# Performance work log

Measured on AMD Instinct MI355X. Metric: run time of the kernel, lower is better.

The kernel has to match this reference:

```python
import jax, jax.numpy as jnp
import numpy as np

TAU = 2.0
BN_EPS = 1e-5


def ms_lif(x_seq, v_th):
    # Multi-step LIF: v <- v + (x - v)/tau; spike = H(v - v_th); hard reset to 0.
    def step(v, x):
        v = v + (x - v) / TAU
        s = (v >= v_th).astype(x.dtype)
        v = v * (1.0 - s)
        return v, s
    _, spikes = jax.lax.scan(step, jnp.zeros_like(x_seq[0]), x_seq)
    return spikes


def conv1x1(x, w):
    # x: [TB, C, H, W], w: [O, C]
    return jnp.einsum('bchw,oc->bohw', x, w)


def bn(x, gamma, beta, mean, var):
    scale = gamma / jnp.sqrt(var + BN_EPS)
    shift = beta - mean * scale
    return x * scale[None, :, None, None] + shift[None, :, None, None]


def setup_inputs() -> dict:
    key = jax.random.key(0)
    ks = jax.random.split(key, 20)
    T, B, C, H, W = 4, 32, 384, 16, 16
    d = {'x': jax.random.normal(ks[0], (T, B, C, H, W), jnp.float32)}
    def bn_params(i):
        return (jax.random.uniform(ks[i], (C,), jnp.float32, 0.5, 1.5),
                jax.random.normal(ks[i + 1], (C,), jnp.float32) * 0.1,
                jax.random.normal(ks[i + 2], (C,), jnp.float32) * 0.1,
                jax.random.uniform(ks[i + 3], (C,), jnp.float32, 0.5, 1.5))
    d['q_w'] = jax.random.normal(ks[1], (C, C), jnp.float32) * (C ** -0.5)
    d['q_gamma'], d['q_beta'], d['q_mean'], d['q_var'] = bn_params(2)
    d['k_w'] = jax.random.normal(ks[6], (C, C), jnp.float32) * (C ** -0.5)
    d['k_gamma'], d['k_beta'], d['k_mean'], d['k_var'] = bn_params(7)
    d['v_w'] = jax.random.normal(ks[11], (C, C), jnp.float32) * (C ** -0.5)
    d['v_gamma'], d['v_beta'], d['v_mean'], d['v_var'] = bn_params(12)
    d['proj_w'] = jax.random.normal(ks[16], (C, C), jnp.float32) * (C ** -0.5)
    d['proj_b'] = jnp.zeros((C,), jnp.float32)
    d['proj_gamma'], d['proj_beta'], d['proj_mean'], d['proj_var'] = bn_params(16)
    return d


def reference(x, q_w, q_gamma, q_beta, q_mean, q_var,
              k_w, k_gamma, k_beta, k_mean, k_var,
              v_w, v_gamma, v_beta, v_mean, v_var,
              proj_w, proj_b, proj_gamma, proj_beta, proj_mean, proj_var):
    T, B, C, H, W = x.shape
    nh = 8
    dh = C // nh
    N = H * W
    identity = x
    xs = ms_lif(x, 1.0)                        # shortcut_lif
    xf = xs.reshape(T * B, C, H, W)

    def branch(w, g, b, m, v_):
        y = bn(conv1x1(xf, w), g, b, m, v_).reshape(T, B, C, H, W)
        return ms_lif(y, 1.0)

    def to_heads(s):  # [T,B,C,H,W] -> [T,B,nh,N,dh]
        return s.reshape(T, B, C, N).transpose(0, 1, 3, 2).reshape(T, B, N, nh, dh).transpose(0, 1, 3, 2, 4)

    q = to_heads(branch(q_w, q_gamma, q_beta, q_mean, q_var))
    k = to_heads(branch(k_w, k_gamma, k_beta, k_mean, k_var))
    v = to_heads(branch(v_w, v_gamma, v_beta, v_mean, v_var))

    kv = (k * v).sum(axis=-2, keepdims=True)   # [T,B,nh,1,dh]
    kv = ms_lif(kv, 0.5)                       # talking_heads_lif (v_th=0.5)
    y = q * kv                                 # [T,B,nh,N,dh]
    y = y.transpose(0, 1, 2, 4, 3).reshape(T * B, C, H, W)
    out = conv1x1(y, proj_w) + proj_b[None, :, None, None]
    out = bn(out, proj_gamma, proj_beta, proj_mean, proj_var).reshape(T, B, C, H, W)
    out = out + identity
    return out, v
```

## Files before the change

### kernel.cpp

```cpp
#include <hip/hip_runtime.h>

#define T_ 4
#define B_ 32
#define C_ 384
#define N_ 256
#define NH_ 8
#define DH_ 48
#define CG_ 48
#define WELE_ 147456
#define FRAGS_M_ 442368
#define ELEMS_ ((size_t)T_*B_*C_*N_)

typedef __bf16 bf16x8 __attribute__((ext_vector_type(8)));
typedef float  f32x4  __attribute__((ext_vector_type(4)));
typedef unsigned int u32x4 __attribute__((ext_vector_type(4)));
typedef unsigned int u32x2 __attribute__((ext_vector_type(2)));
typedef unsigned short u16;

__device__ __forceinline__ float bf2f(u16 h){
  unsigned u = ((unsigned)h) << 16;
  return __builtin_bit_cast(float, u);
}
__device__ __forceinline__ u16 f2bf(float f){
  unsigned u = __builtin_bit_cast(unsigned, f);
  u += 0x7FFFu + ((u >> 16) & 1u);
  return (u16)(u >> 16);
}

__global__ __launch_bounds__(256) void k0_split(
    const float* __restrict__ wq, const float* __restrict__ wk,
    const float* __restrict__ wv, const float* __restrict__ wp,
    u16* __restrict__ ws)
{
  const int m = blockIdx.y;
  const int tid = blockIdx.x * 256 + threadIdx.x;
  const float* W = (m == 0) ? wq : (m == 1) ? wk : (m == 2) ? wv : wp;
  const int fo   = tid / 768;
  const int rem  = tid % 768;
  const int k32  = rem / 64;
  const int lane = rem % 64;
  const int row  = fo*16 + (lane & 15);
  const int col  = k32*32 + (lane >> 4)*8;
  const float* src = W + (size_t)row*C_ + col;

  u16 hi8[8], mi8[8], lo8[8];
#pragma unroll
  for (int e = 0; e < 8; e++){
    float w = src[e];
    u16 hi = f2bf(w);  float r1 = w  - bf2f(hi);
    u16 mi = f2bf(r1); float r2 = r1 - bf2f(mi);
    u16 lo = f2bf(r2);
    hi8[e] = hi; mi8[e] = mi; lo8[e] = lo;
  }
  u16* dst = ws + (size_t)m*FRAGS_M_ + (size_t)((fo*12 + k32)*3)*512 + (size_t)lane*8;
  u32x4 pk;
#pragma unroll
  for (int p = 0; p < 3; p++){
    const u16* s = (p == 0) ? hi8 : (p == 1) ? mi8 : lo8;
    pk[0] = (unsigned)s[0] | ((unsigned)s[1] << 16);
    pk[1] = (unsigned)s[2] | ((unsigned)s[3] << 16);
    pk[2] = (unsigned)s[4] | ((unsigned)s[5] << 16);
    pk[3] = (unsigned)s[6] | ((unsigned)s[7] << 16);
    *(u32x4*)(dst + (size_t)p*512) = pk;
  }
}

__global__ __launch_bounds__(256) void k1_lif_in(const float* __restrict__ x, u16* __restrict__ xs)
{
  const int b = blockIdx.x, cg = blockIdx.y, n = threadIdx.x;
  const int c0 = cg * 8;
  float v[8];
#pragma unroll
  for (int i = 0; i < 8; i++) v[i] = 0.f;
#pragma unroll
  for (int t = 0; t < T_; t++){
    const float* xp = x + (((size_t)(t*B_ + b))*C_ + c0)*N_ + n;
    u16 sp[8];
#pragma unroll
    for (int i = 0; i < 8; i++){
      float xv = xp[(size_t)i * N_];
      float vv = v[i] + (xv - v[i]) * 0.5f;
      bool s = vv >= 1.0f;
      sp[i] = s ? (u16)0x3F80u : (u16)0u;
      v[i] = s ? 0.f : vv;
    }
    u32x4 pk;
    pk[0] = (unsigned)sp[0] | ((unsigned)sp[1] << 16);
    pk[1] = (unsigned)sp[2] | ((unsigned)sp[3] << 16);
    pk[2] = (unsigned)sp[4] | ((unsigned)sp[5] << 16);
    pk[3] = (unsigned)sp[6] | ((unsigned)sp[7] << 16);
    *(u32x4*)(xs + ((size_t)((t*B_ + b)*CG_ + cg))*2048 + (size_t)n*8) = pk;
  }
}

__global__ __launch_bounds__(256) void k2_branch(
    const u16* __restrict__ xs, const u16* __restrict__ wsplit,
    const float* __restrict__ gq, const float* __restrict__ beq, const float* __restrict__ mq, const float* __restrict__ vaq,
    const float* __restrict__ gk, const float* __restrict__ bek, const float* __restrict__ mk, const float* __restrict__ vak,
    const float* __restrict__ gv, const float* __restrict__ bev, const float* __restrict__ mv, const float* __restrict__ vav,
    u16* __restrict__ qspk, u16* __restrict__ kspk, u16* __restrict__ vspk)
{
  const int id   = blockIdx.x;
  const int xcd  = id & 7;
  const int rest = id >> 3;
  const int obi  = rest % 18;
  const int nb4  = (rest / 18) & 3;
  const int bloc = rest / 72;
  const int b    = xcd * 4 + bloc;
  const int ob   = obi * 64;
  const int nb   = nb4 * 64;

  const int lane = threadIdx.x & 63;
  const int w    = __builtin_amdgcn_readfirstlane((int)(threadIdx.x >> 6));
  const int wo = w & 1, wn = w >> 1;
  const int l15 = lane & 15, lg = lane >> 4;
  const int branch = ob / C_;
  const int obr = (ob % C_) + wo * 32;
  const int fo  = obr >> 4;

  const float *G, *Be, *M, *Va; u16* spdst;
  if (branch == 0){ G=gq; Be=beq; M=mq; Va=vaq; spdst=qspk; }
  else if (branch == 1){ G=gk; Be=bek; M=mk; Va=vak; spdst=kspk; }
  else { G=gv; Be=bev; M=mv; Va=vav; spdst=vspk; }

  const int nbl = nb + wn * 32;

  const u16* wb0 = wsplit + (size_t)branch*FRAGS_M_ + (size_t)(fo*36)*512;
  const u16* wb1 = wb0 + (size_t)36*512;
  const u16* xb0 = xs + (size_t)((0*B_ + b)*CG_)*2048;
  const u16* xb1 = xs + (size_t)((1*B_ + b)*CG_)*2048;
  const u16* xb2 = xs + (size_t)((2*B_ + b)*CG_)*2048;
  const u16* xb3 = xs + (size_t)((3*B_ + b)*CG_)*2048;
  const unsigned woff = (unsigned)lane * 8;
  const unsigned xoff = (unsigned)(lg*2048 + (nbl + l15)*8);

  f32x4 acc[T_][2][2];
#pragma unroll
  for (int t = 0; t < T_; t++)
#pragma unroll
    for (int io = 0; io < 2; io++)
#pragma unroll
      for (int in = 0; in < 2; in++) acc[t][io][in] = (f32x4){0.f,0.f,0.f,0.f};

#pragma unroll
  for (int k = 0; k < 12; k++){
    bf16x8 wf[2][3];
    wf[0][0] = *(const bf16x8*)(wb0 + woff);
    wf[0][1] = *(const bf16x8*)(wb0 + woff + 512);
    wf[0][2] = *(const bf16x8*)(wb0 + woff + 1024);
    wf[1][0] = *(const bf16x8*)(wb1 + woff);
    wf[1][1] = *(const bf16x8*)(wb1 + woff + 512);
    wf[1][2] = *(const bf16x8*)(wb1 + woff + 1024);

    bf16x8 bb[T_][2];
    bb[0][0] = *(const bf16x8*)(xb0 + xoff);
    bb[0][1] = *(const bf16x8*)(xb0 + xoff + 128);
    bb[1][0] = *(const bf16x8*)(xb1 + xoff);
    bb[1][1] = *(const bf16x8*)(xb1 + xoff + 128);
    bb[2][0] = *(const bf16x8*)(xb2 + xoff);
    bb[2][1] = *(const bf16x8*)(xb2 + xoff + 128);
    bb[3][0] = *(const bf16x8*)(xb3 + xoff);
    bb[3][1] = *(const bf16x8*)(xb3 + xoff + 128);

#pragma unroll
    for (int t = 0; t < T_; t++)
#pragma unroll
      for (int in = 0; in < 2; in++){
        acc[t][0][in] = __builtin_amdgcn_mfma_f32_16x16x32_bf16(wf[0][2], bb[t][in], acc[t][0][in], 0, 0, 0);
        acc[t][0][in] = __builtin_amdgcn_mfma_f32_16x16x32_bf16(wf[0][1], bb[t][in], acc[t][0][in], 0, 0, 0);
        acc[t][0][in] = __builtin_amdgcn_mfma_f32_16x16x32_bf16(wf[0][0], bb[t][in], acc[t][0][in], 0, 0, 0);
        acc[t][1][in] = __builtin_amdgcn_mfma_f32_16x16x32_bf16(wf[1][2], bb[t][in], acc[t][1][in], 0, 0, 0);
        acc[t][1][in] = __builtin_amdgcn_mfma_f32_16x16x32_bf16(wf[1][1], bb[t][in], acc[t][1][in], 0, 0, 0);
        acc[t][1][in] = __builtin_amdgcn_mfma_f32_16x16x32_bf16(wf[1][0], bb[t][in], acc[t][1][in], 0, 0, 0);
      }

    wb0 += 1536; wb1 += 1536;
    xb0 += 8192; xb1 += 8192; xb2 += 8192; xb3 += 8192;
  }

  float sc[2][4], sh[2][4];
#pragma unroll
  for (int io = 0; io < 2; io++)
#pragma unroll
    for (int j = 0; j < 4; j++){
      int o = obr + io*16 + lg*4 + j;
      float s = G[o] / sqrtf(Va[o] + 1e-5f);
      sc[io][j] = s;
      sh[io][j] = Be[o] - __fmul_rn(M[o], s);
    }

  float vm[2][2][4];
#pragma unroll
  for (int io = 0; io < 2; io++)
#pragma unroll
    for (int in = 0; in < 2; in++)
#pragma unroll
      for (int j = 0; j < 4; j++) vm[io][in][j] = 0.f;

#pragma unroll
  for (int t = 0; t < T_; t++){
#pragma unroll
    for (int io = 0; io < 2; io++)
#pragma unroll
      for (int in = 0; in < 2; in++){
        int n = nbl + in*16 + l15;
        u16 sp[4];
#pragma unroll
        for (int j = 0; j < 4; j++){
          float z = __fadd_rn(__fmul_rn(acc[t][io][in][j], sc[io][j]), sh[io][j]);
          float vv = vm[io][in][j];
          vv = vv + (z - vv) * 0.5f;
          bool s = vv >= 1.0f;
          sp[j] = s ? (u16)0x3F80u : (u16)0u;
          vm[io][in][j] = s ? 0.f : vv;
        }
        u32x2 pk;
        pk[0] = (unsigned)sp[0] | ((unsigned)sp[1] << 16);
        pk[1] = (unsigned)sp[2] | ((unsigned)sp[3] << 16);
        int od = obr + io*16 + lg*4;
        u16* dst = spdst + (size_t)((t*B_ + b)*CG_ + (od >> 3))*2048 + (size_t)n*8 + (od & 7);
        *(u32x2*)dst = pk;
      }
  }
}

__global__ __launch_bounds__(256) void k3_kv(
    const u16* __restrict__ kspk, const u16* __restrict__ vspk, u16* __restrict__ kvm)
{
  const int wid  = (int)((blockIdx.x * blockDim.x + threadIdx.x) >> 6);
  const int lane = threadIdx.x & 63;
  const int b = wid / CG_, cg = wid % CG_;
  float u[8];
#pragma unroll
  for (int i = 0; i < 8; i++) u[i] = 0.f;

#pragma unroll
  for (int t = 0; t < T_; t++){
    int cnt[8];
#pragma unroll
    for (int i = 0; i < 8; i++) cnt[i] = 0;
    const size_t rowoff = (size_t)((t*B_ + b)*CG_ + cg)*2048;
    const u16* kp = kspk + rowoff;
    const u16* vp = vspk + rowoff;
#pragma unroll
    for (int j = 0; j < 4; j++){
      int n = j*64 + lane;
      u32x4 kk = *(const u32x4*)(kp + (size_t)n*8);
      u32x4 vv = *(const u32x4*)(vp + (size_t)n*8);
#pragma unroll
      for (int wd = 0; wd < 4; wd++){
        unsigned both = kk[wd] & vv[wd];
        cnt[2*wd]   += (both & 0xFFFFu) ? 1 : 0;
        cnt[2*wd+1] += (both >> 16)     ? 1 : 0;
      }
    }
#pragma unroll
    for (int i = 0; i < 8; i++){
#pragma unroll
      for (int off = 32; off >= 1; off >>= 1) cnt[i] += __shfl_xor(cnt[i], off, 64);
    }
    u16 mk[8];
#pragma unroll
    for (int i = 0; i < 8; i++){
      float kvf = (float)cnt[i];
      float uu = u[i] + (kvf - u[i]) * 0.5f;
      bool s = uu >= 0.5f;
      mk[i] = s ? (u16)0xFFFFu : (u16)0u;
      u[i] = s ? 0.f : uu;
    }
    if (lane == 0){
      u32x4 pk;
      pk[0] = (unsigned)mk[0] | ((unsigned)mk[1] << 16);
      pk[1] = (unsigned)mk[2] | ((unsigned)mk[3] << 16);
      pk[2] = (unsigned)mk[4] | ((unsigned)mk[5] << 16);
      pk[3] = (unsigned)mk[6] | ((unsigned)mk[7] << 16);
      *(u32x4*)(kvm + (size_t)(t*B_ + b)*C_ + cg*8) = pk;
    }
  }
}

__global__ __launch_bounds__(256) void k5_vtrans(const u16* __restrict__ vspk, float* __restrict__ vout)
{
  const int tb = blockIdx.x, h = blockIdx.y;
  const u16* src = vspk + ((size_t)tb*CG_ + h*6)*2048;
  float* dst = vout + ((size_t)tb*NH_ + h)*(N_*DH_);
#pragma unroll
  for (int i = 0; i < 12; i++){
    int f = i*1024 + threadIdx.x*4;
    int n = f / DH_;
    int d = f - n*DH_;
    u32x2 rv = *(const u32x2*)(src + (size_t)(d >> 3)*2048 + (size_t)n*8 + (d & 7));
    f32x4 o;
    o[0] = (rv[0] & 0xFFFFu) ? 1.f : 0.f;
    o[1] = (rv[0] >> 16)     ? 1.f : 0.f;
    o[2] = (rv[1] & 0xFFFFu) ? 1.f : 0.f;
    o[3] = (rv[1] >> 16)     ? 1.f : 0.f;
    *(f32x4*)(dst + f) = o;
  }
}

__global__ __launch_bounds__(256) void k4_proj(
    const u16* __restrict__ qspk, const u16* __restrict__ kvm, const u16* __restrict__ wsplit,
    const float* __restrict__ pb,
    const float* __restrict__ gp, const float* __restrict__ bep,
    const float* __restrict__ mp, const float* __restrict__ vap,
    const float* __restrict__ x, float* __restrict__ out)
{
  const int id   = blockIdx.x;
  const int xcd  = id & 7;
  const int rest = id >> 3;
  const int obi  = rest % 6;
  const int nb2  = (rest / 6) & 1;
  const int tbl  = rest / 12;
  const int tb   = xcd * 16 + tbl;
  const int ob   = obi * 64;
  const int nb   = nb2 * 128;

  __shared__ __align__(16) u16 kvmask[C_];
  for (int i = threadIdx.x; i < C_; i += 256) kvmask[i] = kvm[(size_t)tb*C_ + i];
  __syncthreads();

  const int lane = threadIdx.x & 63;
  const int w    = __builtin_amdgcn_readfirstlane((int)(threadIdx.x >> 6));
  const int wo = w & 1, wn = w >> 1;
  const int l15 = lane & 15, lg = lane >> 4;
  const int obw = ob + wo * 32;
  const int fo  = obw >> 4;
  const int nbl = nb + wn * 64;

  const u16* wb0 = wsplit + (size_t)3*FRAGS_M_ + (size_t)(fo*36)*512;
  const u16* wb1 = wb0 + (size_t)36*512;
  const u16* qb  = qspk + (size_t)(tb*CG_)*2048;
  const unsigned woff = (unsigned)lane * 8;
  const unsigned qoff = (unsigned)(lg*2048 + (nbl + l15)*8);

  float sc[2][4], sh[2][4], pbv[2][4];
#pragma unroll
  for (int io = 0; io < 2; io++)
#pragma unroll
    for (int j = 0; j < 4; j++){
      int o = obw + io*16 + lg*4 + j;
      float s = gp[o] / sqrtf(vap[o] + 1e-5f);
      sc[io][j] = s;
      sh[io][j] = bep[o] - __fmul_rn(mp[o], s);
      pbv[io][j] = pb[o];
    }

  f32x4 acc[2][4];
#pragma unroll
  for (int io = 0; io < 2; io++)
#pragma unroll
    for (int in = 0; in < 4; in++) acc[io][in] = (f32x4){0.f,0.f,0.f,0.f};

#pragma unroll
  for (int k = 0; k < 12; k++){
    bf16x8 a0 = *(const bf16x8*)(wb0 + woff);
    bf16x8 a1 = *(const bf16x8*)(wb1 + woff);
    u32x4 mv = *(const u32x4*)&kvmask[k*32 + lg*8];
    bf16x8 bb[4];
#pragma unroll
    for (int in = 0; in < 4; in++){
      u32x4 qv = *(const u32x4*)(qb + qoff + in*128);
      u32x4 yv = qv & mv;
      bb[in] = __builtin_bit_cast(bf16x8, yv);
    }
#pragma unroll
    for (int in = 0; in < 4; in++){
      acc[0][in] = __builtin_amdgcn_mfma_f32_16x16x32_bf16(a0, bb[in], acc[0][in], 0, 0, 0);
      acc[1][in] = __builtin_amdgcn_mfma_f32_16x16x32_bf16(a1, bb[in], acc[1][in], 0, 0, 0);
    }
    wb0 += 1536; wb1 += 1536;
    qb  += 8192;
  }

#pragma unroll
  for (int io = 0; io < 2; io++)
#pragma unroll
    for (int in = 0; in < 4; in++){
      int n = nbl + in*16 + l15;
#pragma unroll
      for (int j = 0; j < 4; j++){
        int o = obw + io*16 + lg*4 + j;
        size_t off = ((size_t)tb*C_ + o)*N_ + n;
        float z = __fadd_rn(acc[io][in][j], pbv[io][j]);
        z = __fmul_rn(z, sc[io][j]);
        z = __fadd_rn(z, sh[io][j]);
        z = __fadd_rn(z, x[off]);
        out[off] = z;
      }
    }
}

extern "C" void kernel_launch(void* const* d_in, const int* in_sizes, int n_in,
                              void* d_out, int out_size, void* d_ws, size_t ws_size,
                              hipStream_t stream)
{
  (void)in_sizes; (void)n_in; (void)out_size; (void)ws_size;
  const float* x   = (const float*)d_in[0];
  const float* qw  = (const float*)d_in[1];
  const float* qg  = (const float*)d_in[2];
  const float* qbe = (const float*)d_in[3];
  const float* qm  = (const float*)d_in[4];
  const float* qva = (const float*)d_in[5];
  const float* kw  = (const float*)d_in[6];
  const float* kg  = (const float*)d_in[7];
  const float* kbe = (const float*)d_in[8];
  const float* km  = (const float*)d_in[9];
  const float* kva = (const float*)d_in[10];
  const float* vw  = (const float*)d_in[11];
  const float* vg  = (const float*)d_in[12];
  const float* vbe = (const float*)d_in[13];
  const float* vm  = (const float*)d_in[14];
  const float* vva = (const float*)d_in[15];
  const float* pw  = (const float*)d_in[16];
  const float* pb  = (const float*)d_in[17];
  const float* pg  = (const float*)d_in[18];
  const float* pbe = (const float*)d_in[19];
  const float* pm  = (const float*)d_in[20];
  const float* pva = (const float*)d_in[21];

  float* out  = (float*)d_out;
  float* vout = out + ELEMS_;

  u16* vspk = (u16*)d_out;

  u16* wsplit = (u16*)d_ws;
  u16* xs   = wsplit + (size_t)4*FRAGS_M_;
  u16* qspk = xs   + ELEMS_;
  u16* kspk = qspk + ELEMS_;
  u16* kvm  = kspk + ELEMS_;

  k0_split<<<dim3(72, 4), 256, 0, stream>>>(qw, kw, vw, pw, wsplit);
  k1_lif_in<<<dim3(B_, CG_), 256, 0, stream>>>(x, xs);
  k2_branch<<<dim3(2304), 256, 0, stream>>>(xs, wsplit,
      qg, qbe, qm, qva,
      kg, kbe, km, kva,
      vg, vbe, vm, vva,
      qspk, kspk, vspk);
  k3_kv<<<dim3(384), 256, 0, stream>>>(kspk, vspk, kvm);
  k5_vtrans<<<dim3(T_*B_, NH_), 256, 0, stream>>>(vspk, vout);
  k4_proj<<<dim3(1536), 256, 0, stream>>>(qspk, kvm, wsplit,
      pb, pg, pbe, pm, pva, x, out);
}
```

Baseline: 145.7 us.

## Stage spike activations through double-buffered LDS with async global-to-LDS loads

New measurement: 140.3 us. 1.04x faster.

```diff
diff --git a/kernel.cpp b/kernel.cpp
--- a/kernel.cpp
+++ b/kernel.cpp
@@ -26,6 +26,11 @@
   u += 0x7FFFu + ((u >> 16) & 1u);
   return (u16)(u >> 16);
 }
+__device__ __forceinline__ void gl_lds16(const u16* g, u16* l){
+  __builtin_amdgcn_global_load_lds(
+      (const __attribute__((address_space(1))) void*)g,
+      (__attribute__((address_space(3))) void*)l, 16, 0, 0);
+}
 
 __global__ __launch_bounds__(256) void k0_split(
     const float* __restrict__ wq, const float* __restrict__ wk,
@@ -100,6 +105,8 @@
     const float* __restrict__ gv, const float* __restrict__ bev, const float* __restrict__ mv, const float* __restrict__ vav,
     u16* __restrict__ qspk, u16* __restrict__ kspk, u16* __restrict__ vspk)
 {
+  __shared__ __align__(16) u16 sbuf[2][8192];
+
   const int id   = blockIdx.x;
   const int xcd  = id & 7;
   const int rest = id >> 3;
@@ -127,12 +134,12 @@
 
   const u16* wb0 = wsplit + (size_t)branch*FRAGS_M_ + (size_t)(fo*36)*512;
   const u16* wb1 = wb0 + (size_t)36*512;
-  const u16* xb0 = xs + (size_t)((0*B_ + b)*CG_)*2048;
-  const u16* xb1 = xs + (size_t)((1*B_ + b)*CG_)*2048;
-  const u16* xb2 = xs + (size_t)((2*B_ + b)*CG_)*2048;
-  const u16* xb3 = xs + (size_t)((3*B_ + b)*CG_)*2048;
   const unsigned woff = (unsigned)lane * 8;
-  const unsigned xoff = (unsigned)(lg*2048 + (nbl + l15)*8);
+
+  const u16* gstage = xs + (size_t)((w*B_ + b)*CG_)*2048 + (size_t)nb*8 + (size_t)lane*8;
+  u16* lstage = &sbuf[0][0] + (unsigned)(w*4*512);
+
+  const unsigned roff = (unsigned)(lg*512 + wn*256 + l15*8);
 
   f32x4 acc[T_][2][2];
 #pragma unroll
@@ -143,39 +150,65 @@
       for (int in = 0; in < 2; in++) acc[t][io][in] = (f32x4){0.f,0.f,0.f,0.f};
 
 #pragma unroll
+  for (int cg = 0; cg < 4; cg++)
+    gl_lds16(gstage + cg*2048, lstage + cg*512);
+  bf16x8 wfc[2][3];
+  wfc[0][0] = *(const bf16x8*)(wb0 + woff);
+  wfc[0][1] = *(const bf16x8*)(wb0 + woff + 512);
+  wfc[0][2] = *(const bf16x8*)(wb0 + woff + 1024);
+  wfc[1][0] = *(const bf16x8*)(wb1 + woff);
+  wfc[1][1] = *(const bf16x8*)(wb1 + woff + 512);
+  wfc[1][2] = *(const bf16x8*)(wb1 + woff + 1024);
+  __syncthreads();
+
+  int buf = 0;
+#pragma unroll
   for (int k = 0; k < 12; k++){
-    bf16x8 wf[2][3];
-    wf[0][0] = *(const bf16x8*)(wb0 + woff);
-    wf[0][1] = *(const bf16x8*)(wb0 + woff + 512);
-    wf[0][2] = *(const bf16x8*)(wb0 + woff + 1024);
-    wf[1][0] = *(const bf16x8*)(wb1 + woff);
-    wf[1][1] = *(const bf16x8*)(wb1 + woff + 512);
-    wf[1][2] = *(const bf16x8*)(wb1 + woff + 1024);
-
-    bf16x8 bb[T_][2];
-    bb[0][0] = *(const bf16x8*)(xb0 + xoff);
-    bb[0][1] = *(const bf16x8*)(xb0 + xoff + 128);
-    bb[1][0] = *(const bf16x8*)(xb1 + xoff);
-    bb[1][1] = *(const bf16x8*)(xb1 + xoff + 128);
-    bb[2][0] = *(const bf16x8*)(xb2 + xoff);
-    bb[2][1] = *(const bf16x8*)(xb2 + xoff + 128);
-    bb[3][0] = *(const bf16x8*)(xb3 + xoff);
-    bb[3][1] = *(const bf16x8*)(xb3 + xoff + 128);
-
-#pragma unroll
-    for (int t = 0; t < T_; t++)
-#pragma unroll
-      for (int in = 0; in < 2; in++){
-        acc[t][0][in] = __builtin_amdgcn_mfma_f32_16x16x32_bf16(wf[0][2], bb[t][in], acc[t][0][in], 0, 0, 0);
-        acc[t][0][in] = __builtin_amdgcn_mfma_f32_16x16x32_bf16(wf[0][1], bb[t][in], acc[t][0][in], 0, 0, 0);
-        acc[t][0][in] = __builtin_amdgcn_mfma_f32_16x16x32_bf16(wf[0][0], bb[t][in], acc[t][0][in], 0, 0, 0);
-        acc[t][1][in] = __builtin_amdgcn_mfma_f32_16x16x32_bf16(wf[1][2], bb[t][in], acc[t][1][in], 0, 0, 0);
-        acc[t][1][in] = __builtin_amdgcn_mfma_f32_16x16x32_bf16(wf[1][1], bb[t][in], acc[t][1][in], 0, 0, 0);
-        acc[t][1][in] = __builtin_amdgcn_mfma_f32_16x16x32_bf16(wf[1][0], bb[t][in], acc[t][1][in], 0, 0, 0);
-      }
-
+    bf16x8 wfn[2][3];
+    if (k < 11){
+      const u16* gs = gstage + (size_t)(k+1)*8192;
+      u16* ls = lstage + (unsigned)((buf^1)*8192);
+#pragma unroll
+      for (int cg = 0; cg < 4; cg++)
+        gl_lds16(gs + cg*2048, ls + cg*512);
+      wfn[0][0] = *(const bf16x8*)(wb0 + woff + 1536);
+      wfn[0][1] = *(const bf16x8*)(wb0 + woff + 2048);
+      wfn[0][2] = *(const bf16x8*)(wb0 + woff + 2560);
+      wfn[1][0] = *(const bf16x8*)(wb1 + woff + 1536);
+      wfn[1][1] = *(const bf16x8*)(wb1 + woff + 2048);
+      wfn[1][2] = *(const bf16x8*)(wb1 + woff + 2560);
+    }
+
+    const u16* sb = &sbuf[buf][0];
+#pragma unroll
+    for (int tp = 0; tp < 4; tp += 2){
+      bf16x8 bb[2][2];
+      bb[0][0] = *(const bf16x8*)(sb + (unsigned)(tp  )*2048 + roff);
+      bb[0][1] = *(const bf16x8*)(sb + (unsigned)(tp  )*2048 + roff + 128);
+      bb[1][0] = *(const bf16x8*)(sb + (unsigned)(tp+1)*2048 + roff);
+      bb[1][1] = *(const bf16x8*)(sb + (unsigned)(tp+1)*2048 + roff + 128);
+#pragma unroll
+      for (int tt = 0; tt < 2; tt++)
+#pragma unroll
+        for (int in = 0; in < 2; in++){
+          acc[tp+tt][0][in] = __builtin_amdgcn_mfma_f32_16x16x32_bf16(wfc[0][2], bb[tt][in], acc[tp+tt][0][in], 0, 0, 0);
+          acc[tp+tt][0][in] = __builtin_amdgcn_mfma_f32_16x16x32_bf16(wfc[0][1], bb[tt][in], acc[tp+tt][0][in], 0, 0, 0);
+          acc[tp+tt][0][in] = __builtin_amdgcn_mfma_f32_16x16x32_bf16(wfc[0][0], bb[tt][in], acc[tp+tt][0][in], 0, 0, 0);
+          acc[tp+tt][1][in] = __builtin_amdgcn_mfma_f32_16x16x32_bf16(wfc[1][2], bb[tt][in], acc[tp+tt][1][in], 0, 0, 0);
+          acc[tp+tt][1][in] = __builtin_amdgcn_mfma_f32_16x16x32_bf16(wfc[1][1], bb[tt][in], acc[tp+tt][1][in], 0, 0, 0);
+          acc[tp+tt][1][in] = __builtin_amdgcn_mfma_f32_16x16x32_bf16(wfc[1][0], bb[tt][in], acc[tp+tt][1][in], 0, 0, 0);
+        }
+    }
+
+    __syncthreads();
+    if (k < 11){
+#pragma unroll
+      for (int io = 0; io < 2; io++)
+#pragma unroll
+        for (int p = 0; p < 3; p++) wfc[io][p] = wfn[io][p];
+    }
     wb0 += 1536; wb1 += 1536;
-    xb0 += 8192; xb1 += 8192; xb2 += 8192; xb3 += 8192;
+    buf ^= 1;
   }
 
   float sc[2][4], sh[2][4];
```
